# Performance work log

Hardware: AMD Instinct MI355X
Metric: run time of the kernel (lower is better)

## Reference

```python
import jax, jax.numpy as jnp
import numpy as np
from jax import lax

T, B, D, H = 512, 2048, 64, 10  # time, batch, input_dim, hidden_dim (= n_qubits)
CLIP = 5.0


def setup_inputs() -> dict:
    key = jax.random.key(0)
    ks = jax.random.split(key, 5)
    inputs = jax.random.normal(ks[0], (T, B, D), jnp.float32)

    def lin(k):
        kw, kb = jax.random.split(k)
        W = jax.random.normal(kw, (H, D + H), jnp.float32) * 0.1
        b = jax.random.normal(kb, (H,), jnp.float32) * 0.1
        return W, b

    Wf, bf = lin(ks[1])
    Wi, bi = lin(ks[2])
    Wu, bu = lin(ks[3])
    Wo, bo = lin(ks[4])
    return dict(inputs=inputs, Wf=Wf, bf=bf, Wi=Wi, bi=bi,
                Wu=Wu, bu=bu, Wo=Wo, bo=bo)


def _quantum_gate(p):
    # Analytic statevector result: RX(p_q) per qubit then CX chain q->q+1.
    # <Z_q> = prod_{j<=q} cos(p_j); Qiskit big-endian labels reverse the order.
    return jnp.flip(jnp.cumprod(jnp.cos(p), axis=-1), axis=-1)


def _fcl(hx):
    # RY(hx_q) per qubit, measure Z on qubit n-1 (label 'Z'+'I'*(n-1)) -> cos(hx[:, -1])
    return jnp.cos(hx[:, -1:])  # [B, 1]


def reference(inputs, Wf, bf, Wi, bi, Wu, bu, Wo, bo):
    Bsz = inputs.shape[1]
    Hd = Wf.shape[0]
    h0 = jnp.zeros((Bsz, Hd), inputs.dtype)
    c0 = jnp.zeros((Bsz, Hd), inputs.dtype)

    def step(carry, x):
        hx, cx = carry
        comb = jnp.concatenate([x, hx], axis=1)  # [B, D+H]
        clip = lambda z: jnp.clip(z, -CLIP, CLIP)
        f = jax.nn.sigmoid(_quantum_gate(clip(comb @ Wf.T + bf)))
        i = jax.nn.sigmoid(_quantum_gate(clip(comb @ Wi.T + bi)))
        g = jnp.tanh(_quantum_gate(clip(comb @ Wu.T + bu)))
        o = jax.nn.sigmoid(_quantum_gate(clip(comb @ Wo.T + bo)))
        cx = f * cx + i * g
        hx = o * jnp.tanh(cx)
        hx = hx * _fcl(hx)  # scalar modulation broadcast over hidden dim
        return (hx, cx), hx

    (hx, cx), outputs = lax.scan(step, (h0, c0), inputs)
    return outputs, (hx, cx)
```

## Files before the change

### kernel.cpp

```cpp
#include <hip/hip_runtime.h>

#define TT    512
#define BATCH 2048
#define DIN   64
#define HD    10
#define WROW  (DIN + HD)
#define NGATE 40
#define ZSTRIDE (BATCH * NGATE)
#define ZNEED ((size_t)(TT + 4) * ZSTRIDE * 4)

__global__ __launch_bounds__(256, 2)
void zgemm_kernel(const float* __restrict__ X,
                  const float* __restrict__ Wf, const float* __restrict__ bf,
                  const float* __restrict__ Wi, const float* __restrict__ bi,
                  const float* __restrict__ Wu, const float* __restrict__ bu,
                  const float* __restrict__ Wo, const float* __restrict__ bo,
                  float* __restrict__ Z)
{
    const int tid  = threadIdx.x;
    const int n    = tid & 63;
    const int msub = tid >> 6;
    __shared__ float xs[16][64];

    float w[DIN];
    float bias = 0.f;
    {
        const float* Wg = Wf; const float* bg = bf;
        const int g = n / HD;
        if (g == 1) { Wg = Wi; bg = bi; }
        else if (g == 2) { Wg = Wu; bg = bu; }
        else if (g == 3) { Wg = Wo; bg = bo; }
        const int q = n - g * HD;
        if (n < NGATE) {
            #pragma unroll
            for (int k = 0; k < DIN; ++k) w[k] = Wg[q * WROW + k];
            bias = bg[q];
        } else {
            #pragma unroll
            for (int k = 0; k < DIN; ++k) w[k] = 0.f;
        }
    }

    const size_t m0 = (size_t)blockIdx.x * 64;
    #pragma unroll 1
    for (int c = 0; c < 4; ++c) {
        const size_t mc = m0 + (size_t)c * 16;
        __syncthreads();
        {
            const float4 xv = *reinterpret_cast<const float4*>(&X[mc * DIN + (size_t)tid * 4]);
            *reinterpret_cast<float4*>(&xs[0][0] + tid * 4) = xv;
        }
        __syncthreads();
        #pragma unroll
        for (int j = 0; j < 4; ++j) {
            const int ml = msub * 4 + j;
            float s0 = bias, s1 = 0.f, s2 = 0.f, s3 = 0.f;
            #pragma unroll
            for (int k = 0; k < DIN; k += 4) {
                float4 xq = *reinterpret_cast<const float4*>(&xs[ml][k]);
                s0 = fmaf(w[k + 0], xq.x, s0);
                s1 = fmaf(w[k + 1], xq.y, s1);
                s2 = fmaf(w[k + 2], xq.z, s2);
                s3 = fmaf(w[k + 3], xq.w, s3);
            }
            if (n < NGATE) Z[(mc + ml) * NGATE + n] = (s0 + s1) + (s2 + s3);
        }
    }
}

__global__ __launch_bounds__(64, 2)
void qlstm_rec_kernel(const float* __restrict__ Z,
                      const float* __restrict__ Wf, const float* __restrict__ Wi,
                      const float* __restrict__ Wu, const float* __restrict__ Wo,
                      float* __restrict__ out)
{
    const int row  = blockIdx.x;
    const int lane = threadIdx.x;
    const int g    = lane >> 4;
    const int v    = lane & 15;
    const bool act_lane = (v >= 6);

    const float LOG2E  = 1.4426950408889634f;
    const float INV2PI = 0.15915494309189535f;

    float cmul = -LOG2E, amul = 1.f, aadd = 0.f;
    const float* Wg = Wf;
    if (g == 1) { Wg = Wi; }
    else if (g == 2) { Wg = Wu; cmul = -2.f * LOG2E; amul = 2.f; aadd = -1.f; }
    else if (g == 3) { Wg = Wo; }

    float wh[HD];
    if (act_lane) {
        const int uw = 15 - v;
        #pragma unroll
        for (int k = 0; k < HD; ++k) wh[k] = Wg[uw * WROW + DIN + k];
    } else {
        #pragma unroll
        for (int k = 0; k < HD; ++k) wh[k] = 0.f;
    }

    int n = g * HD + (15 - v);
    if (n > NGATE - 1) n = NGATE - 1;
    const float* Zp = Z + (size_t)row * NGATE + n;

    float h[HD];
    #pragma unroll
    for (int k = 0; k < HD; ++k) h[k] = 0.f;
    float c = 0.f;
    float hkeep = 0.f;

    float z0 = Zp[0];
    float z1 = Zp[(size_t)ZSTRIDE];
    float z2 = Zp[(size_t)2 * ZSTRIDE];

    #pragma unroll 1
    for (int t = 0; t < TT; ++t) {
        const float zx = z0;
        z0 = z1; z1 = z2;
        z2 = Zp[(size_t)(t + 3) * ZSTRIDE];

        float za = zx, zb = 0.f;
        #pragma unroll
        for (int j = 0; j < HD; j += 2) {
            za = fmaf(wh[j],     h[j],     za);
            zb = fmaf(wh[j + 1], h[j + 1], zb);
        }
        float z = za + zb;
        z = fminf(fmaxf(z, -5.f), 5.f);
        float p = __builtin_amdgcn_cosf(z * INV2PI);

        {
            int s_;
            s_ = __builtin_amdgcn_update_dpp(0x3f800000, __float_as_int(p), 0x101, 0xF, 0xF, false);
            p *= __int_as_float(s_);
            s_ = __builtin_amdgcn_update_dpp(0x3f800000, __float_as_int(p), 0x102, 0xF, 0xF, false);
            p *= __int_as_float(s_);
            s_ = __builtin_amdgcn_update_dpp(0x3f800000, __float_as_int(p), 0x104, 0xF, 0xF, false);
            p *= __int_as_float(s_);
            s_ = __builtin_amdgcn_update_dpp(0x3f800000, __float_as_int(p), 0x108, 0xF, 0xF, false);
            p *= __int_as_float(s_);
        }

        float e = __builtin_amdgcn_exp2f(cmul * p);
        float a = amul * __builtin_amdgcn_rcpf(1.f + e) + aadd;

        float fg = __shfl(a, v);
        float ig = __shfl(a, 16 + v);
        float ug = __shfl(a, 32 + v);
        float og = __shfl(a, 48 + v);

        c = fmaf(fg, c, ig * ug);
        float e2 = __builtin_amdgcn_exp2f(-2.f * LOG2E * c);
        float th = 2.f * __builtin_amdgcn_rcpf(1.f + e2) - 1.f;
        float hpre = og * th;
        float h9 = __int_as_float(__builtin_amdgcn_readlane(__float_as_int(hpre), 15));
        float m  = __builtin_amdgcn_cosf(h9 * INV2PI);
        float hnew = hpre * m;
        hkeep = hnew;

        if (lane >= 6 && lane < 16) out[((size_t)t * BATCH + row) * HD + (lane - 6)] = hnew;

        #pragma unroll
        for (int j = 0; j < HD; ++j)
            h[j] = __int_as_float(__builtin_amdgcn_readlane(__float_as_int(hnew), 6 + j));
    }

    if (lane >= 6 && lane < 16) {
        const size_t base = (size_t)TT * BATCH * HD;
        out[base + (size_t)row * HD + (lane - 6)] = hkeep;
        out[base + (size_t)BATCH * HD + (size_t)row * HD + (lane - 6)] = c;
    }
}

__global__ __launch_bounds__(64, 2)
void qlstm_fused_kernel(const float* __restrict__ X,
                        const float* __restrict__ Wf, const float* __restrict__ bf,
                        const float* __restrict__ Wi, const float* __restrict__ bi,
                        const float* __restrict__ Wu, const float* __restrict__ bu,
                        const float* __restrict__ Wo, const float* __restrict__ bo,
                        float* __restrict__ out)
{
    const int row  = blockIdx.x;
    const int lane = threadIdx.x;
    const int g    = lane >> 4;
    const int v    = lane & 15;
    const bool act_lane = (v >= 6);

    __shared__ float xs[2][DIN];

    const float LOG2E  = 1.4426950408889634f;
    const float INV2PI = 0.15915494309189535f;

    float cmul = -LOG2E, amul = 1.f, aadd = 0.f;
    const float* Wg = Wf; const float* bg = bf;
    if (g == 1) { Wg = Wi; bg = bi; }
    else if (g == 2) { Wg = Wu; bg = bu; cmul = -2.f * LOG2E; amul = 2.f; aadd = -1.f; }
    else if (g == 3) { Wg = Wo; bg = bo; }

    float wx[DIN];
    float wh[HD];
    float bias = 0.f;
    if (act_lane) {
        const int uw = 15 - v;
        #pragma unroll
        for (int k = 0; k < DIN; ++k) wx[k] = Wg[uw * WROW + k];
        #pragma unroll
        for (int k = 0; k < HD; ++k)  wh[k] = Wg[uw * WROW + DIN + k];
        bias = bg[uw];
    } else {
        #pragma unroll
        for (int k = 0; k < DIN; ++k) wx[k] = 0.f;
        #pragma unroll
        for (int k = 0; k < HD; ++k)  wh[k] = 0.f;
    }

    float h[HD];
    #pragma unroll
    for (int k = 0; k < HD; ++k) h[k] = 0.f;
    float c = 0.f;
    float hkeep = 0.f;

    const size_t xstep = (size_t)BATCH * DIN;
    const size_t xbase = (size_t)row * DIN + lane;

    xs[0][lane] = X[xbase];
    float xr = X[xstep + xbase];

    float zx;
    {
        float s0 = bias, s1 = 0.f, s2 = 0.f, s3 = 0.f;
        #pragma unroll
        for (int k = 0; k < DIN; k += 4) {
            float4 xq = *reinterpret_cast<const float4*>(&xs[0][k]);
            s0 = fmaf(wx[k + 0], xq.x, s0);
            s1 = fmaf(wx[k + 1], xq.y, s1);
            s2 = fmaf(wx[k + 2], xq.z, s2);
            s3 = fmaf(wx[k + 3], xq.w, s3);
        }
        zx = (s0 + s1) + (s2 + s3);
    }

    int cur = 0;
    for (int t = 0; t < TT; ++t) {
        const int nxt = cur ^ 1;
        if (t + 1 < TT) xs[nxt][lane] = xr;
        if (t + 2 < TT) xr = X[(size_t)(t + 2) * xstep + xbase];

        float za = zx, zb = 0.f;
        #pragma unroll
        for (int j = 0; j < HD; j += 2) {
            za = fmaf(wh[j],     h[j],     za);
            zb = fmaf(wh[j + 1], h[j + 1], zb);
        }
        float z = za + zb;
        z = fminf(fmaxf(z, -5.f), 5.f);
        float p = __builtin_amdgcn_cosf(z * INV2PI);

        {
            int s_;
            s_ = __builtin_amdgcn_update_dpp(0x3f800000, __float_as_int(p), 0x101, 0xF, 0xF, false);
            p *= __int_as_float(s_);
            s_ = __builtin_amdgcn_update_dpp(0x3f800000, __float_as_int(p), 0x102, 0xF, 0xF, false);
            p *= __int_as_float(s_);
            s_ = __builtin_amdgcn_update_dpp(0x3f800000, __float_as_int(p), 0x104, 0xF, 0xF, false);
            p *= __int_as_float(s_);
            s_ = __builtin_amdgcn_update_dpp(0x3f800000, __float_as_int(p), 0x108, 0xF, 0xF, false);
            p *= __int_as_float(s_);
        }

        float e = __builtin_amdgcn_exp2f(cmul * p);
        float a = amul * __builtin_amdgcn_rcpf(1.f + e) + aadd;

        float fg = __shfl(a, v);
        float ig = __shfl(a, 16 + v);
        float ug = __shfl(a, 32 + v);
        float og = __shfl(a, 48 + v);

        c = fmaf(fg, c, ig * ug);
        float e2 = __builtin_amdgcn_exp2f(-2.f * LOG2E * c);
        float th = 2.f * __builtin_amdgcn_rcpf(1.f + e2) - 1.f;
        float hpre = og * th;
        float h9 = __int_as_float(__builtin_amdgcn_readlane(__float_as_int(hpre), 15));
        float m  = __builtin_amdgcn_cosf(h9 * INV2PI);
        float hnew = hpre * m;
        hkeep = hnew;

        if (lane >= 6 && lane < 16) out[((size_t)t * BATCH + row) * HD + (lane - 6)] = hnew;

        #pragma unroll
        for (int j = 0; j < HD; ++j)
            h[j] = __int_as_float(__builtin_amdgcn_readlane(__float_as_int(hnew), 6 + j));

        if (t + 1 < TT) {
            float s0 = bias, s1 = 0.f, s2 = 0.f, s3 = 0.f;
            const float* xp = xs[nxt];
            #pragma unroll
            for (int k = 0; k < DIN; k += 4) {
                float4 xq = *reinterpret_cast<const float4*>(&xp[k]);
                s0 = fmaf(wx[k + 0], xq.x, s0);
                s1 = fmaf(wx[k + 1], xq.y, s1);
                s2 = fmaf(wx[k + 2], xq.z, s2);
                s3 = fmaf(wx[k + 3], xq.w, s3);
            }
            zx = (s0 + s1) + (s2 + s3);
        }
        cur = nxt;
    }

    if (lane >= 6 && lane < 16) {
        const size_t base = (size_t)TT * BATCH * HD;
        out[base + (size_t)row * HD + (lane - 6)] = hkeep;
        out[base + (size_t)BATCH * HD + (size_t)row * HD + (lane - 6)] = c;
    }
}

extern "C" void kernel_launch(void* const* d_in, const int* in_sizes, int n_in,
                              void* d_out, int out_size, void* d_ws, size_t ws_size,
                              hipStream_t stream) {
    const float* X  = (const float*)d_in[0];
    const float* Wf = (const float*)d_in[1];
    const float* bf = (const float*)d_in[2];
    const float* Wi = (const float*)d_in[3];
    const float* bi = (const float*)d_in[4];
    const float* Wu = (const float*)d_in[5];
    const float* bu = (const float*)d_in[6];
    const float* Wo = (const float*)d_in[7];
    const float* bo = (const float*)d_in[8];
    float* out = (float*)d_out;

    if (ws_size >= ZNEED) {
        float* Zbuf = (float*)d_ws;
        zgemm_kernel<<<(TT * BATCH) / 64, 256, 0, stream>>>(
            X, Wf, bf, Wi, bi, Wu, bu, Wo, bo, Zbuf);
        qlstm_rec_kernel<<<BATCH, 64, 0, stream>>>(Zbuf, Wf, Wi, Wu, Wo, out);
    } else {
        qlstm_fused_kernel<<<BATCH, 64, 0, stream>>>(
            X, Wf, bf, Wi, bi, Wu, bu, Wo, bo, out);
    }
}
```

Measured before the change: 711.6 us.

## Rework input GEMM to per-wave row streaming and unroll recurrence by four

The input-projection kernel drops shared-memory staging and barriers. Each wavefront now owns a contiguous run of 64 rows and reads X directly, with the row index made wave-uniform so the loads can be scalar or broadcast, and it launches a fixed grid of 4096 blocks with a higher occupancy hint. The recurrent kernel unrolls the time loop by four through a macro, keeps a four-deep Z prefetch, replaces __shfl with ds_bpermute using precomputed byte addresses, and uses a pointer that advances for output stores. The aim is to cut LDS and sync overhead in the GEMM and loop and indexing overhead in the latency-bound recurrence, at the risk of more register pressure and per-lane redundant global loads.

```diff
diff --git a/kernel.cpp b/kernel.cpp
--- a/kernel.cpp
+++ b/kernel.cpp
@@ -9,7 +9,7 @@
 #define ZSTRIDE (BATCH * NGATE)
 #define ZNEED ((size_t)(TT + 4) * ZSTRIDE * 4)
 
-__global__ __launch_bounds__(256, 2)
+__global__ __launch_bounds__(256, 4)
 void zgemm_kernel(const float* __restrict__ X,
                   const float* __restrict__ Wf, const float* __restrict__ bf,
                   const float* __restrict__ Wi, const float* __restrict__ bi,
@@ -17,54 +17,48 @@
                   const float* __restrict__ Wo, const float* __restrict__ bo,
                   float* __restrict__ Z)
 {
-    const int tid  = threadIdx.x;
-    const int n    = tid & 63;
-    const int msub = tid >> 6;
-    __shared__ float xs[16][64];
+    const int lane = threadIdx.x & 63;
+    int wid = blockIdx.x * 4 + (threadIdx.x >> 6);
+    wid = __builtin_amdgcn_readfirstlane(wid);
 
     float w[DIN];
     float bias = 0.f;
-    {
-        const float* Wg = Wf; const float* bg = bf;
-        const int g = n / HD;
-        if (g == 1) { Wg = Wi; bg = bi; }
-        else if (g == 2) { Wg = Wu; bg = bu; }
-        else if (g == 3) { Wg = Wo; bg = bo; }
-        const int q = n - g * HD;
-        if (n < NGATE) {
-            #pragma unroll
-            for (int k = 0; k < DIN; ++k) w[k] = Wg[q * WROW + k];
-            bias = bg[q];
-        } else {
-            #pragma unroll
-            for (int k = 0; k < DIN; ++k) w[k] = 0.f;
-        }
-    }
-
-    const size_t m0 = (size_t)blockIdx.x * 64;
+    if (lane < NGATE) {
+        const int g = lane / HD;
+        const int u = lane - g * HD;
+        const float* Wg = (g == 0) ? Wf : (g == 1) ? Wi : (g == 2) ? Wu : Wo;
+        const float* bg = (g == 0) ? bf : (g == 1) ? bi : (g == 2) ? bu : bo;
+        const float2* wr = reinterpret_cast<const float2*>(Wg + u * WROW);
+        #pragma unroll
+        for (int k2 = 0; k2 < DIN / 2; ++k2) {
+            float2 tv = wr[k2];
+            w[2 * k2]     = tv.x;
+            w[2 * k2 + 1] = tv.y;
+        }
+        bias = bg[u];
+    } else {
+        #pragma unroll
+        for (int k = 0; k < DIN; ++k) w[k] = 0.f;
+    }
+
+    const int ROWS = (TT * BATCH) / (4096 * 4);
+    size_t m = (size_t)wid * ROWS;
+    const float* xr = X + m * DIN;
+    float* zp = Z + m * NGATE;
+
     #pragma unroll 1
-    for (int c = 0; c < 4; ++c) {
-        const size_t mc = m0 + (size_t)c * 16;
-        __syncthreads();
-        {
-            const float4 xv = *reinterpret_cast<const float4*>(&X[mc * DIN + (size_t)tid * 4]);
-            *reinterpret_cast<float4*>(&xs[0][0] + tid * 4) = xv;
-        }
-        __syncthreads();
-        #pragma unroll
-        for (int j = 0; j < 4; ++j) {
-            const int ml = msub * 4 + j;
-            float s0 = bias, s1 = 0.f, s2 = 0.f, s3 = 0.f;
-            #pragma unroll
-            for (int k = 0; k < DIN; k += 4) {
-                float4 xq = *reinterpret_cast<const float4*>(&xs[ml][k]);
-                s0 = fmaf(w[k + 0], xq.x, s0);
-                s1 = fmaf(w[k + 1], xq.y, s1);
-                s2 = fmaf(w[k + 2], xq.z, s2);
-                s3 = fmaf(w[k + 3], xq.w, s3);
-            }
-            if (n < NGATE) Z[(mc + ml) * NGATE + n] = (s0 + s1) + (s2 + s3);
-        }
+    for (int r = 0; r < ROWS; ++r) {
+        float s0 = bias, s1 = 0.f, s2 = 0.f, s3 = 0.f;
+        #pragma unroll
+        for (int k = 0; k < DIN; k += 4) {
+            s0 = fmaf(w[k + 0], xr[k + 0], s0);
+            s1 = fmaf(w[k + 1], xr[k + 1], s1);
+            s2 = fmaf(w[k + 2], xr[k + 2], s2);
+            s3 = fmaf(w[k + 3], xr[k + 3], s3);
+        }
+        if (lane < NGATE) zp[lane] = (s0 + s1) + (s2 + s3);
+        xr += DIN;
+        zp += NGATE;
     }
 }
 
@@ -103,67 +97,78 @@
     if (n > NGATE - 1) n = NGATE - 1;
     const float* Zp = Z + (size_t)row * NGATE + n;
 
+    const int ba0 = v * 4;
+    const int ba1 = (16 + v) * 4;
+    const int ba2 = (32 + v) * 4;
+    const int ba3 = (48 + v) * 4;
+
     float h[HD];
     #pragma unroll
     for (int k = 0; k < HD; ++k) h[k] = 0.f;
     float c = 0.f;
     float hkeep = 0.f;
 
-    float z0 = Zp[0];
-    float z1 = Zp[(size_t)ZSTRIDE];
-    float z2 = Zp[(size_t)2 * ZSTRIDE];
+    float* op = out + (size_t)row * HD + (lane - 6);
+
+    float zfa = Zp[(size_t)0 * ZSTRIDE];
+    float zfb = Zp[(size_t)1 * ZSTRIDE];
+    float zfc = Zp[(size_t)2 * ZSTRIDE];
+    float zfd = Zp[(size_t)3 * ZSTRIDE];
+
+#define QSTEP(ZREG, TNEXT)                                                              \
+    {                                                                                   \
+        const float zx = ZREG;                                                          \
+        ZREG = Zp[(size_t)(TNEXT) * ZSTRIDE];                  \
+        float za = zx, zb = 0.f;                                                        \
+        _Pragma("unroll")                                                               \
+        for (int j = 0; j < HD; j += 2) {                                               \
+            za = fmaf(wh[j],     h[j],     za);                                         \
+            zb = fmaf(wh[j + 1], h[j + 1], zb);                                         \
+        }                                                                               \
+        float z = za + zb;                                                              \
+        z = fminf(fmaxf(z, -5.f), 5.f);                                                 \
+        float p = __builtin_amdgcn_cosf(z * INV2PI);                                    \
+        {                                                                               \
+            int s_;                                                                     \
+            s_ = __builtin_amdgcn_update_dpp(0x3f800000, __float_as_int(p), 0x101, 0xF, 0xF, false); \
+            p *= __int_as_float(s_);                                                    \
+            s_ = __builtin_amdgcn_update_dpp(0x3f800000, __float_as_int(p), 0x102, 0xF, 0xF, false); \
+            p *= __int_as_float(s_);                                                    \
+            s_ = __builtin_amdgcn_update_dpp(0x3f800000, __float_as_int(p), 0x104, 0xF, 0xF, false); \
+            p *= __int_as_float(s_);                                                    \
+            s_ = __builtin_amdgcn_update_dpp(0x3f800000, __float_as_int(p), 0x108, 0xF, 0xF, false); \
+            p *= __int_as_float(s_);                                                    \
+        }                                                                               \
+        float e = __builtin_amdgcn_exp2f(cmul * p);                                     \
+        float a = amul * __builtin_amdgcn_rcpf(1.f + e) + aadd;                         \
+        const int ai = __float_as_int(a);                                               \
+        float fg = __int_as_float(__builtin_amdgcn_ds_bpermute(ba0, ai));               \
+        float ig = __int_as_float(__builtin_amdgcn_ds_bpermute(ba1, ai));               \
+        float ug = __int_as_float(__builtin_amdgcn_ds_bpermute(ba2, ai));               \
+        float og = __int_as_float(__builtin_amdgcn_ds_bpermute(ba3, ai));               \
+        c = fmaf(fg, c, ig * ug);                                                       \
+        float e2 = __builtin_amdgcn_exp2f(-2.f * LOG2E * c);                            \
+        float th = 2.f * __builtin_amdgcn_rcpf(1.f + e2) - 1.f;                         \
+        float hpre = og * th;                                                           \
+        float h9 = __int_as_float(__builtin_amdgcn_readlane(__float_as_int(hpre), 15)); \
+        float m_ = __builtin_amdgcn_cosf(h9 * INV2PI);                                  \
+        float hnew = hpre * m_;                                                         \
+        hkeep = hnew;                                                                   \
+        if (lane >= 6 && lane < 16) *op = hnew;                                         \
+        op += (size_t)BATCH * HD;                                                       \
+        _Pragma("unroll")                                                               \
+        for (int j = 0; j < HD; ++j)                                                    \
+            h[j] = __int_as_float(__builtin_amdgcn_readlane(__float_as_int(hnew), 6 + j)); \
+    }
 
     #pragma unroll 1
-    for (int t = 0; t < TT; ++t) {
-        const float zx = z0;
-        z0 = z1; z1 = z2;
-        z2 = Zp[(size_t)(t + 3) * ZSTRIDE];
-
-        float za = zx, zb = 0.f;
-        #pragma unroll
-        for (int j = 0; j < HD; j += 2) {
-            za = fmaf(wh[j],     h[j],     za);
-            zb = fmaf(wh[j + 1], h[j + 1], zb);
-        }
-        float z = za + zb;
-        z = fminf(fmaxf(z, -5.f), 5.f);
-        float p = __builtin_amdgcn_cosf(z * INV2PI);
-
-        {
-            int s_;
-            s_ = __builtin_amdgcn_update_dpp(0x3f800000, __float_as_int(p), 0x101, 0xF, 0xF, false);
-            p *= __int_as_float(s_);
-            s_ = __builtin_amdgcn_update_dpp(0x3f800000, __float_as_int(p), 0x102, 0xF, 0xF, false);
-            p *= __int_as_float(s_);
-            s_ = __builtin_amdgcn_update_dpp(0x3f800000, __float_as_int(p), 0x104, 0xF, 0xF, false);
-            p *= __int_as_float(s_);
-            s_ = __builtin_amdgcn_update_dpp(0x3f800000, __float_as_int(p), 0x108, 0xF, 0xF, false);
-            p *= __int_as_float(s_);
-        }
-
-        float e = __builtin_amdgcn_exp2f(cmul * p);
-        float a = amul * __builtin_amdgcn_rcpf(1.f + e) + aadd;
-
-        float fg = __shfl(a, v);
-        float ig = __shfl(a, 16 + v);
-        float ug = __shfl(a, 32 + v);
-        float og = __shfl(a, 48 + v);
-
-        c = fmaf(fg, c, ig * ug);
-        float e2 = __builtin_amdgcn_exp2f(-2.f * LOG2E * c);
-        float th = 2.f * __builtin_amdgcn_rcpf(1.f + e2) - 1.f;
-        float hpre = og * th;
-        float h9 = __int_as_float(__builtin_amdgcn_readlane(__float_as_int(hpre), 15));
-        float m  = __builtin_amdgcn_cosf(h9 * INV2PI);
-        float hnew = hpre * m;
-        hkeep = hnew;
-
-        if (lane >= 6 && lane < 16) out[((size_t)t * BATCH + row) * HD + (lane - 6)] = hnew;
-
-        #pragma unroll
-        for (int j = 0; j < HD; ++j)
-            h[j] = __int_as_float(__builtin_amdgcn_readlane(__float_as_int(hnew), 6 + j));
-    }
+    for (int t = 0; t < TT; t += 4) {
+        QSTEP(zfa, t + 4)
+        QSTEP(zfb, t + 5)
+        QSTEP(zfc, t + 6)
+        QSTEP(zfd, t + 7)
+    }
+#undef QSTEP
 
     if (lane >= 6 && lane < 16) {
         const size_t base = (size_t)TT * BATCH * HD;
@@ -281,7 +286,7 @@
         float th = 2.f * __builtin_amdgcn_rcpf(1.f + e2) - 1.f;
         float hpre = og * th;
         float h9 = __int_as_float(__builtin_amdgcn_readlane(__float_as_int(hpre), 15));
-        float m  = __builtin_amdgcn_cosf(h9 * INV2PI);
+        float m = __builtin_amdgcn_cosf(h9 * INV2PI);
         float hnew = hpre * m;
         hkeep = hnew;
 
@@ -330,7 +335,7 @@
 
     if (ws_size >= ZNEED) {
         float* Zbuf = (float*)d_ws;
-        zgemm_kernel<<<(TT * BATCH) / 64, 256, 0, stream>>>(
+        zgemm_kernel<<<4096, 256, 0, stream>>>(
             X, Wf, bf, Wi, bi, Wu, bu, Wo, bo, Zbuf);
         qlstm_rec_kernel<<<BATCH, 64, 0, stream>>>(Zbuf, Wf, Wi, Wu, Wo, out);
     } else {
```

New measurement: 880.8 us. 1.24x slower.

## Compute all four gates per lane with interleaved Z layout in recurrence

Applied to the files above, without the earlier changes.

The Z buffer is re-laid out so the four gate pre-activations for each hidden unit sit contiguously, letting each lane load them with one float4. The recurrent kernel now evaluates all four gates in each lane, which removes the four cross-lane shuffles per step, and folds the cos modulation into the next step's matvec through the factor m. The time loop is unrolled by four with a four-deep prefetch. In exchange each lane does four times the matvec and transcendental work and holds 40 weight registers, which may raise register pressure.

```diff
diff --git a/kernel.cpp b/kernel.cpp
--- a/kernel.cpp
+++ b/kernel.cpp
@@ -6,8 +6,9 @@
 #define HD    10
 #define WROW  (DIN + HD)
 #define NGATE 40
-#define ZSTRIDE (BATCH * NGATE)
-#define ZNEED ((size_t)(TT + 4) * ZSTRIDE * 4)
+#define ZROW  40
+#define ZSLAB ((size_t)BATCH * ZROW)
+#define ZNEED ((size_t)(TT + 4) * ZSLAB * 4)
 
 __global__ __launch_bounds__(256, 2)
 void zgemm_kernel(const float* __restrict__ X,
@@ -24,6 +25,7 @@
 
     float w[DIN];
     float bias = 0.f;
+    int zcol = 0;
     {
         const float* Wg = Wf; const float* bg = bf;
         const int g = n / HD;
@@ -35,6 +37,7 @@
             #pragma unroll
             for (int k = 0; k < DIN; ++k) w[k] = Wg[q * WROW + k];
             bias = bg[q];
+            zcol = q * 4 + g;
         } else {
             #pragma unroll
             for (int k = 0; k < DIN; ++k) w[k] = 0.f;
@@ -63,7 +66,7 @@
                 s2 = fmaf(w[k + 2], xq.z, s2);
                 s3 = fmaf(w[k + 3], xq.w, s3);
             }
-            if (n < NGATE) Z[(mc + ml) * NGATE + n] = (s0 + s1) + (s2 + s3);
+            if (n < NGATE) Z[(mc + ml) * ZROW + zcol] = (s0 + s1) + (s2 + s3);
         }
     }
 }
@@ -76,94 +79,109 @@
 {
     const int row  = blockIdx.x;
     const int lane = threadIdx.x;
-    const int g    = lane >> 4;
     const int v    = lane & 15;
-    const bool act_lane = (v >= 6);
+    int uw = 15 - v; if (uw > 9) uw = 9;
 
     const float LOG2E  = 1.4426950408889634f;
     const float INV2PI = 0.15915494309189535f;
 
-    float cmul = -LOG2E, amul = 1.f, aadd = 0.f;
-    const float* Wg = Wf;
-    if (g == 1) { Wg = Wi; }
-    else if (g == 2) { Wg = Wu; cmul = -2.f * LOG2E; amul = 2.f; aadd = -1.f; }
-    else if (g == 3) { Wg = Wo; }
-
-    float wh[HD];
-    if (act_lane) {
-        const int uw = 15 - v;
-        #pragma unroll
-        for (int k = 0; k < HD; ++k) wh[k] = Wg[uw * WROW + DIN + k];
-    } else {
-        #pragma unroll
-        for (int k = 0; k < HD; ++k) wh[k] = 0.f;
-    }
-
-    int n = g * HD + (15 - v);
-    if (n > NGATE - 1) n = NGATE - 1;
-    const float* Zp = Z + (size_t)row * NGATE + n;
+    float whf[HD], whi[HD], whu[HD], who[HD];
+    #pragma unroll
+    for (int j = 0; j < HD; ++j) {
+        whf[j] = Wf[uw * WROW + DIN + j];
+        whi[j] = Wi[uw * WROW + DIN + j];
+        whu[j] = Wu[uw * WROW + DIN + j];
+        who[j] = Wo[uw * WROW + DIN + j];
+    }
+
+    const float4* Zp = reinterpret_cast<const float4*>(
+        Z + (size_t)row * ZROW + (size_t)uw * 4);
+    const size_t ZS4 = (size_t)BATCH * (ZROW / 4);
 
     float h[HD];
     #pragma unroll
-    for (int k = 0; k < HD; ++k) h[k] = 0.f;
-    float c = 0.f;
-    float hkeep = 0.f;
-
-    float z0 = Zp[0];
-    float z1 = Zp[(size_t)ZSTRIDE];
-    float z2 = Zp[(size_t)2 * ZSTRIDE];
+    for (int j = 0; j < HD; ++j) h[j] = 0.f;
+    float c = 0.f, m = 1.f, hkeep = 0.f;
+
+    float* op = out + (size_t)row * HD + (lane - 6);
+
+    float4 za = Zp[0];
+    float4 zb = Zp[ZS4];
+    float4 zc = Zp[2 * ZS4];
+    float4 zd = Zp[3 * ZS4];
+
+#define QSTEP(ZQ, TNEXT)                                                                \
+    {                                                                                   \
+        const float4 zq = ZQ;                                                           \
+        ZQ = Zp[(size_t)(TNEXT) * ZS4];                           \
+        float zhf = 0.f, zhi = 0.f, zhu = 0.f, zho = 0.f;                               \
+        _Pragma("unroll")                                                               \
+        for (int j = 0; j < HD; ++j) {                                                  \
+            zhf = fmaf(whf[j], h[j], zhf);                                              \
+            zhi = fmaf(whi[j], h[j], zhi);                                              \
+            zhu = fmaf(whu[j], h[j], zhu);                                              \
+            zho = fmaf(who[j], h[j], zho);                                              \
+        }                                                                               \
+        float zf = fmaf(m, zhf, zq.x);                                                  \
+        float zi = fmaf(m, zhi, zq.y);                                                  \
+        float zu = fmaf(m, zhu, zq.z);                                                  \
+        float zo = fmaf(m, zho, zq.w);                                                  \
+        zf = fminf(fmaxf(zf, -5.f), 5.f);                                               \
+        zi = fminf(fmaxf(zi, -5.f), 5.f);                                               \
+        zu = fminf(fmaxf(zu, -5.f), 5.f);                                               \
+        zo = fminf(fmaxf(zo, -5.f), 5.f);                                               \
+        float pf = __builtin_amdgcn_cosf(zf * INV2PI);                                  \
+        float pi_ = __builtin_amdgcn_cosf(zi * INV2PI);                                 \
+        float pu = __builtin_amdgcn_cosf(zu * INV2PI);                                  \
+        float po = __builtin_amdgcn_cosf(zo * INV2PI);                                  \
+        int s_;                                                                         \
+        s_ = __builtin_amdgcn_update_dpp(0x3f800000, __float_as_int(pf), 0x101, 0xF, 0xF, false); pf *= __int_as_float(s_); \
+        s_ = __builtin_amdgcn_update_dpp(0x3f800000, __float_as_int(pi_), 0x101, 0xF, 0xF, false); pi_ *= __int_as_float(s_); \
+        s_ = __builtin_amdgcn_update_dpp(0x3f800000, __float_as_int(pu), 0x101, 0xF, 0xF, false); pu *= __int_as_float(s_); \
+        s_ = __builtin_amdgcn_update_dpp(0x3f800000, __float_as_int(po), 0x101, 0xF, 0xF, false); po *= __int_as_float(s_); \
+        s_ = __builtin_amdgcn_update_dpp(0x3f800000, __float_as_int(pf), 0x102, 0xF, 0xF, false); pf *= __int_as_float(s_); \
+        s_ = __builtin_amdgcn_update_dpp(0x3f800000, __float_as_int(pi_), 0x102, 0xF, 0xF, false); pi_ *= __int_as_float(s_); \
+        s_ = __builtin_amdgcn_update_dpp(0x3f800000, __float_as_int(pu), 0x102, 0xF, 0xF, false); pu *= __int_as_float(s_); \
+        s_ = __builtin_amdgcn_update_dpp(0x3f800000, __float_as_int(po), 0x102, 0xF, 0xF, false); po *= __int_as_float(s_); \
+        s_ = __builtin_amdgcn_update_dpp(0x3f800000, __float_as_int(pf), 0x104, 0xF, 0xF, false); pf *= __int_as_float(s_); \
+        s_ = __builtin_amdgcn_update_dpp(0x3f800000, __float_as_int(pi_), 0x104, 0xF, 0xF, false); pi_ *= __int_as_float(s_); \
+        s_ = __builtin_amdgcn_update_dpp(0x3f800000, __float_as_int(pu), 0x104, 0xF, 0xF, false); pu *= __int_as_float(s_); \
+        s_ = __builtin_amdgcn_update_dpp(0x3f800000, __float_as_int(po), 0x104, 0xF, 0xF, false); po *= __int_as_float(s_); \
+        s_ = __builtin_amdgcn_update_dpp(0x3f800000, __float_as_int(pf), 0x108, 0xF, 0xF, false); pf *= __int_as_float(s_); \
+        s_ = __builtin_amdgcn_update_dpp(0x3f800000, __float_as_int(pi_), 0x108, 0xF, 0xF, false); pi_ *= __int_as_float(s_); \
+        s_ = __builtin_amdgcn_update_dpp(0x3f800000, __float_as_int(pu), 0x108, 0xF, 0xF, false); pu *= __int_as_float(s_); \
+        s_ = __builtin_amdgcn_update_dpp(0x3f800000, __float_as_int(po), 0x108, 0xF, 0xF, false); po *= __int_as_float(s_); \
+                                       \
+        float ef = __builtin_amdgcn_exp2f(-LOG2E * pf);                                 \
+        float ei = __builtin_amdgcn_exp2f(-LOG2E * pi_);                                \
+        float eu = __builtin_amdgcn_exp2f(-2.f * LOG2E * pu);                           \
+        float eo = __builtin_amdgcn_exp2f(-LOG2E * po);                                 \
+        float gf = __builtin_amdgcn_rcpf(1.f + ef);                                     \
+        float gi = __builtin_amdgcn_rcpf(1.f + ei);                                     \
+        float gu = 2.f * __builtin_amdgcn_rcpf(1.f + eu) - 1.f;                         \
+        float go = __builtin_amdgcn_rcpf(1.f + eo);                                     \
+        c = fmaf(gf, c, gi * gu);                                                       \
+        float e2 = __builtin_amdgcn_exp2f(-2.f * LOG2E * c);                            \
+        float th = 2.f * __builtin_amdgcn_rcpf(1.f + e2) - 1.f;                         \
+        float hpre = go * th;                                                           \
+        _Pragma("unroll")                                                               \
+        for (int j = 0; j < HD; ++j)                                                    \
+            h[j] = __int_as_float(__builtin_amdgcn_readlane(__float_as_int(hpre), 6 + j)); \
+        m = __builtin_amdgcn_cosf(h[9] * INV2PI);                                       \
+        float hst = m * hpre;                                                           \
+        hkeep = hst;                                                                    \
+        if (lane >= 6 && lane < 16) *op = hst;                                          \
+        op += (size_t)BATCH * HD;                                                       \
+    }
 
     #pragma unroll 1
-    for (int t = 0; t < TT; ++t) {
-        const float zx = z0;
-        z0 = z1; z1 = z2;
-        z2 = Zp[(size_t)(t + 3) * ZSTRIDE];
-
-        float za = zx, zb = 0.f;
-        #pragma unroll
-        for (int j = 0; j < HD; j += 2) {
-            za = fmaf(wh[j],     h[j],     za);
-            zb = fmaf(wh[j + 1], h[j + 1], zb);
-        }
-        float z = za + zb;
-        z = fminf(fmaxf(z, -5.f), 5.f);
-        float p = __builtin_amdgcn_cosf(z * INV2PI);
-
-        {
-            int s_;
-            s_ = __builtin_amdgcn_update_dpp(0x3f800000, __float_as_int(p), 0x101, 0xF, 0xF, false);
-            p *= __int_as_float(s_);
-            s_ = __builtin_amdgcn_update_dpp(0x3f800000, __float_as_int(p), 0x102, 0xF, 0xF, false);
-            p *= __int_as_float(s_);
-            s_ = __builtin_amdgcn_update_dpp(0x3f800000, __float_as_int(p), 0x104, 0xF, 0xF, false);
-            p *= __int_as_float(s_);
-            s_ = __builtin_amdgcn_update_dpp(0x3f800000, __float_as_int(p), 0x108, 0xF, 0xF, false);
-            p *= __int_as_float(s_);
-        }
-
-        float e = __builtin_amdgcn_exp2f(cmul * p);
-        float a = amul * __builtin_amdgcn_rcpf(1.f + e) + aadd;
-
-        float fg = __shfl(a, v);
-        float ig = __shfl(a, 16 + v);
-        float ug = __shfl(a, 32 + v);
-        float og = __shfl(a, 48 + v);
-
-        c = fmaf(fg, c, ig * ug);
-        float e2 = __builtin_amdgcn_exp2f(-2.f * LOG2E * c);
-        float th = 2.f * __builtin_amdgcn_rcpf(1.f + e2) - 1.f;
-        float hpre = og * th;
-        float h9 = __int_as_float(__builtin_amdgcn_readlane(__float_as_int(hpre), 15));
-        float m  = __builtin_amdgcn_cosf(h9 * INV2PI);
-        float hnew = hpre * m;
-        hkeep = hnew;
-
-        if (lane >= 6 && lane < 16) out[((size_t)t * BATCH + row) * HD + (lane - 6)] = hnew;
-
-        #pragma unroll
-        for (int j = 0; j < HD; ++j)
-            h[j] = __int_as_float(__builtin_amdgcn_readlane(__float_as_int(hnew), 6 + j));
-    }
+    for (int t = 0; t < TT; t += 4) {
+        QSTEP(za, t + 4)
+        QSTEP(zb, t + 5)
+        QSTEP(zc, t + 6)
+        QSTEP(zd, t + 7)
+    }
+#undef QSTEP
 
     if (lane >= 6 && lane < 16) {
         const size_t base = (size_t)TT * BATCH * HD;
@@ -281,7 +299,7 @@
         float th = 2.f * __builtin_amdgcn_rcpf(1.f + e2) - 1.f;
         float hpre = og * th;
         float h9 = __int_as_float(__builtin_amdgcn_readlane(__float_as_int(hpre), 15));
-        float m  = __builtin_amdgcn_cosf(h9 * INV2PI);
+        float m = __builtin_amdgcn_cosf(h9 * INV2PI);
         float hnew = hpre * m;
         hkeep = hnew;
 
```

New measurement: 888.4 us. 24.9% more time.
